# Optimization experiments

Measured on AMD Instinct MI355X. Metric: run time of the kernel, lower is better.

Reference implementation:

```python
import jax, jax.numpy as jnp
import numpy as np

EPS = 1e-5

def batchnorm(x, g, b):
    # training-mode BN: batch statistics over (N,H,W), biased variance (matches torch)
    m = x.mean((0, 2, 3), keepdims=True)
    v = ((x - m) ** 2).mean((0, 2, 3), keepdims=True)
    return g[None, :, None, None] * (x - m) * jax.lax.rsqrt(v + EPS) + b[None, :, None, None]


def deform_conv2d(x, offset, mask, weight, bias):
    # torchvision deform_conv2d v2 semantics, stride=1, pad=1, dilation=1, 1 group, 1 offset group
    B, C, H, W = x.shape
    K = 9  # 3x3 kernel
    off = offset.reshape(B, K, 2, H, W)  # interleaved (dy, dx) per kernel tap
    dy, dx = off[:, :, 0], off[:, :, 1]  # [B,K,H,W]
    kr = jnp.arange(3, dtype=x.dtype) - 1.0
    k_y = jnp.repeat(kr, 3)  # [9] kernel row offsets
    k_x = jnp.tile(kr, 3)    # [9] kernel col offsets
    hh = jnp.arange(H, dtype=x.dtype)
    ww = jnp.arange(W, dtype=x.dtype)
    ph = dy + k_y[None, :, None, None] + hh[None, None, :, None]  # [B,K,H,W] sample rows
    pw = dx + k_x[None, :, None, None] + ww[None, None, None, :]  # [B,K,H,W] sample cols
    h0 = jnp.floor(ph); w0 = jnp.floor(pw)
    lh = ph - h0; lw = pw - w0
    h0i = h0.astype(jnp.int32); w0i = w0.astype(jnp.int32)

    def gather(xb, hb, wb):  # xb [C,H,W], hb/wb [K,H,W] -> [C,K,H,W]
        return xb[:, hb, wb]

    def corner(hi, wi, wgt):
        valid = (hi >= 0) & (hi < H) & (wi >= 0) & (wi < W)
        hic = jnp.clip(hi, 0, H - 1); wic = jnp.clip(wi, 0, W - 1)
        v = jax.vmap(gather)(x, hic, wic)  # [B,C,K,H,W]
        return v * (wgt * valid.astype(x.dtype))[:, None]

    samp = (corner(h0i, w0i, (1 - lh) * (1 - lw))
            + corner(h0i, w0i + 1, (1 - lh) * lw)
            + corner(h0i + 1, w0i, lh * (1 - lw))
            + corner(h0i + 1, w0i + 1, lh * lw))  # [B,C,K,H,W]
    samp = samp * mask[:, None]  # modulated (v2) mask [B,1,K,H,W]
    out = jnp.einsum('bckhw,ock->bohw', samp, weight.reshape(weight.shape[0], C, K))
    return out + bias[None, :, None, None]


def reference(x, conv1_w, bn1_g, bn1_b, off_w, off_b, dcn_w, dcn_b, norm_g, norm_b):
    flip = x[..., ::-1]
    xp = batchnorm(jnp.einsum('bchw,oc->bohw', x, conv1_w), bn1_g, bn1_b)  # 1x1 conv + BN, no relu
    concat = jnp.concatenate([flip, xp], axis=1)  # [B,2C,H,W]
    out = jax.lax.conv_general_dilated(concat, off_w, (1, 1), 'SAME',
                                       dimension_numbers=('NCHW', 'OIHW', 'NCHW'))
    out = out + off_b[None, :, None, None]  # [B,27,H,W]
    o1, o2, mask = jnp.split(out, 3, axis=1)
    offset = jnp.concatenate([o1, o2], axis=1)  # [B,18,H,W]
    mask = jax.nn.sigmoid(mask)  # [B,9,H,W]
    d = deform_conv2d(xp, offset, mask, dcn_w, dcn_b)
    return jax.nn.relu(batchnorm(d, norm_g, norm_b) + xp)


def setup_inputs() -> dict:
    key = jax.random.key(0)
    ks = jax.random.split(key, 6)
    B, C, H, W = 8, 256, 45, 80
    stdv = 1.0 / np.sqrt(C * 9)
    return {
        'x': jax.random.normal(ks[0], (B, C, H, W), jnp.float32),
        'conv1_w': jax.random.normal(ks[1], (C, C), jnp.float32) * 0.05,
        'bn1_g': jnp.ones((C,), jnp.float32),
        'bn1_b': jnp.zeros((C,), jnp.float32),
        'off_w': jax.random.normal(ks[2], (27, 2 * C, 3, 3), jnp.float32) * 0.01,
        'off_b': jax.random.normal(ks[3], (27,), jnp.float32) * 0.01,
        'dcn_w': jax.random.uniform(ks[4], (C, C, 3, 3), jnp.float32, -stdv, stdv),
        'dcn_b': jax.random.normal(ks[5], (C,), jnp.float32) * 0.01,
        'norm_g': jnp.ones((C,), jnp.float32),
        'norm_b': jnp.zeros((C,), jnp.float32),
    }
```

## Files before the change

### kernel.cpp

```cpp
#include <hip/hip_runtime.h>
#include <math.h>

#define BATCH 8
#define CH 256
#define HH 45
#define WW 80
#define HW 3600
#define PTOT 28800

typedef unsigned short u16;
typedef unsigned int   u32;
typedef __attribute__((ext_vector_type(8))) short bf16x8;
typedef __attribute__((ext_vector_type(4))) float f32x4;

struct __align__(8) us4 { u16 x, y, z, w; };

__device__ __forceinline__ u16 bf16_rne(float x) {
  u32 u = __float_as_uint(x);
  u += 0x7FFF + ((u >> 16) & 1);
  return (u16)(u >> 16);
}

__global__ __launch_bounds__(256) void prep_wts(
    const float* __restrict__ conv1_w, const float* __restrict__ off_w,
    const float* __restrict__ dcn_w,
    u16* __restrict__ w1b, u16* __restrict__ wt_offb, u16* __restrict__ wt_b)
{
  int i = blockIdx.x * 256 + threadIdx.x;
  if (i < 256 * 256) {
    w1b[i] = bf16_rne(conv1_w[i]);
  }
  if (i < 9 * 32 * 512) {
    int tap = i >> 14;
    int r   = i & 16383;
    int oc  = r >> 9;
    int c   = r & 511;
    float v = (oc < 27) ? off_w[((size_t)oc * 512 + c) * 9 + tap] : 0.f;
    wt_offb[i] = bf16_rne(v);
  }
  if (i < 9 * 256 * 256) {
    int c = i & 255;
    int oc = (i >> 8) & 255;
    int tap = i >> 16;
    wt_b[i] = bf16_rne(dcn_w[((size_t)oc * 256 + c) * 9 + tap]);
  }
}

__global__ __launch_bounds__(256) void flip_transpose(
    const float* __restrict__ x, u16* __restrict__ concat)
{
  __shared__ float tile[32][36];
  const int b  = blockIdx.z;
  const int c0 = blockIdx.y * 32;
  const int p0 = blockIdx.x * 32;
  int rem = HW - p0; if (rem > 32) rem = 32;
  const int t = threadIdx.x;
  {
    int c = t >> 3, p4 = (t & 7) * 4;
    if (p4 < rem) {
      float4 v = *(const float4*)(x + ((size_t)b * CH + c0 + c) * HW + p0 + p4);
      *(float4*)&tile[c][p4] = v;
    }
  }
  __syncthreads();
  {
    int r = t >> 3, cq = (t & 7) * 4;
    if (r < rem) {
      int p = p0 + r;
      int h = p / WW, w = p - h * WW;
      int pf = h * WW + (WW - 1 - w);
      us4 o;
      o.x = bf16_rne(tile[cq + 0][r]);
      o.y = bf16_rne(tile[cq + 1][r]);
      o.z = bf16_rne(tile[cq + 2][r]);
      o.w = bf16_rne(tile[cq + 3][r]);
      *(us4*)(concat + ((size_t)b * HW + pf) * 512 + c0 + cq) = o;
    }
  }
}

__global__ __launch_bounds__(256) void conv1_mfma(
    const u16* __restrict__ concat, const u16* __restrict__ w1b,
    float* __restrict__ out1)
{
  const int t = threadIdx.x;
  const int wv = t >> 6, lane = t & 63;
  const int lr = lane & 15, lk = lane >> 4;
  const int id = blockIdx.x;
  const int b  = id & 7;
  const int pt = id >> 3;
  const int oc0 = blockIdx.y * 128 + (wv & 1) * 64;
  const int p0  = pt * 128 + (wv >> 1) * 64;

  const u16* bptr[4];
#pragma unroll
  for (int nt = 0; nt < 4; nt++) {
    int pl = p0 + nt * 16 + lr;
    int pc = pl < HW ? pl : HW - 1;
    int h = pc / WW, w = pc - h * WW;
    int pf = b * HW + h * WW + (WW - 1 - w);
    bptr[nt] = concat + (size_t)pf * 512 + lk * 8;
  }
  const u16* aptr = w1b + ((size_t)(oc0 + lr)) * 256 + lk * 8;

  f32x4 acc[4][4];
#pragma unroll
  for (int mt = 0; mt < 4; mt++)
#pragma unroll
    for (int nt = 0; nt < 4; nt++) acc[mt][nt] = (f32x4)0.f;

#pragma unroll
  for (int cc = 0; cc < 8; cc++) {
    bf16x8 af[4], bfv[4];
#pragma unroll
    for (int mt = 0; mt < 4; mt++)
      af[mt] = *(const bf16x8*)(aptr + (size_t)mt * 16 * 256 + cc * 32);
#pragma unroll
    for (int nt = 0; nt < 4; nt++)
      bfv[nt] = *(const bf16x8*)(bptr[nt] + cc * 32);
#pragma unroll
    for (int mt = 0; mt < 4; mt++)
#pragma unroll
      for (int nt = 0; nt < 4; nt++)
        acc[mt][nt] = __builtin_amdgcn_mfma_f32_16x16x32_bf16(
            af[mt], bfv[nt], acc[mt][nt], 0, 0, 0);
  }

#pragma unroll
  for (int mt = 0; mt < 4; mt++) {
    int oc = oc0 + mt * 16 + lk * 4;
#pragma unroll
    for (int nt = 0; nt < 4; nt++) {
      int pl = p0 + nt * 16 + lr;
      if (pl < HW) {
        float* dst = out1 + ((size_t)(b * CH + oc)) * HW + pl;
#pragma unroll
        for (int r = 0; r < 4; r++)
          dst[(size_t)r * HW] = acc[mt][nt][r];
      }
    }
  }
}

__global__ __launch_bounds__(256) void stats_part(
    const float* __restrict__ src, float* __restrict__ part)
{
  const int c = blockIdx.x, b = blockIdx.y;
  const int t = threadIdx.x;
  const float* p = src + ((size_t)b * CH + c) * HW;
  float s = 0.f, s2 = 0.f;
  for (int i = t; i < HW; i += 256) {
    float v = p[i];
    s += v; s2 += v * v;
  }
  __shared__ float ls[256], ls2[256];
  ls[t] = s; ls2[t] = s2;
  __syncthreads();
  for (int off = 128; off > 0; off >>= 1) {
    if (t < off) { ls[t] += ls[t + off]; ls2[t] += ls2[t + off]; }
    __syncthreads();
  }
  if (t == 0) {
    part[((size_t)b * CH + c) * 2]     = ls[0];
    part[((size_t)b * CH + c) * 2 + 1] = ls2[0];
  }
}

__global__ __launch_bounds__(256) void stats_fin(
    const float* __restrict__ part, float* __restrict__ st)
{
  const int c = threadIdx.x;
  float s = 0.f, s2 = 0.f;
#pragma unroll
  for (int b = 0; b < BATCH; b++) {
    s  += part[((size_t)b * CH + c) * 2];
    s2 += part[((size_t)b * CH + c) * 2 + 1];
  }
  float m = s / (float)PTOT;
  float var = s2 / (float)PTOT - m * m;
  st[c] = m;
  st[CH + c] = rsqrtf(var + 1e-5f);
}

__global__ __launch_bounds__(256) void norm_transpose(
    const float* __restrict__ out1, const float* __restrict__ st,
    const float* __restrict__ g, const float* __restrict__ bb,
    u16* __restrict__ concat)
{
  __shared__ float tile[32][36];
  const int b  = blockIdx.z;
  const int c0 = blockIdx.y * 32;
  const int p0 = blockIdx.x * 32;
  int rem = HW - p0; if (rem > 32) rem = 32;
  const int t = threadIdx.x;

  {
    int c  = t >> 3;
    int p4 = (t & 7) * 4;
    int cg = c0 + c;
    float m  = st[cg], rs = st[CH + cg];
    float sc = g[cg] * rs;
    float sh = bb[cg] - m * sc;
    if (p4 < rem) {
      size_t base = ((size_t)b * CH + cg) * HW + p0;
      float4 v = *(const float4*)(out1 + base + p4);
      v.x = v.x * sc + sh; v.y = v.y * sc + sh;
      v.z = v.z * sc + sh; v.w = v.w * sc + sh;
      *(float4*)&tile[c][p4] = v;
    }
  }
  __syncthreads();
  {
    int r  = t >> 3;
    int cq = (t & 7) * 4;
    if (r < rem) {
      us4 o;
      o.x = bf16_rne(tile[cq + 0][r]);
      o.y = bf16_rne(tile[cq + 1][r]);
      o.z = bf16_rne(tile[cq + 2][r]);
      o.w = bf16_rne(tile[cq + 3][r]);
      *(us4*)(concat + ((size_t)b * HW + p0 + r) * 512 + 256 + c0 + cq) = o;
    }
  }
}

__global__ __launch_bounds__(128) void off_mfma(
    const u16* __restrict__ concat, const u16* __restrict__ wt_offb,
    float* __restrict__ offp3)
{
  const int t = threadIdx.x;
  const int g = blockIdx.y;
  const int wv = t >> 6, lane = t & 63;
  const int lr = lane & 15, lk = lane >> 4;
  const int id = blockIdx.x;
  const int b    = id & 7;
  const int tile = id >> 3;
  int pl = tile * 32 + wv * 16 + lr;
  const bool pvalid = pl < HW;
  if (!pvalid) pl = HW - 1;
  const int P = b * HW + pl;
  const int h = pl / WW, w = pl - h * WW;

  f32x4 acc[2];
  acc[0] = (f32x4)0.f; acc[1] = (f32x4)0.f;

#pragma unroll 1
  for (int tl = 0; tl < 3; tl++) {
    int tap = g * 3 + tl;
    int dy = tap / 3 - 1, dx = tap % 3 - 1;
    bool valid = ((unsigned)(h + dy) < HH) && ((unsigned)(w + dx) < WW);
    int Ps = valid ? (P + dy * WW + dx) : P;
    const u16* bp = concat + (size_t)Ps * 512 + lk * 8;
    const u16* ap = wt_offb + ((size_t)tap * 32 + lr) * 512 + lk * 8;
#pragma unroll
    for (int cc = 0; cc < 16; cc++) {
      bf16x8 bfv = *(const bf16x8*)(bp + cc * 32);
      if (!valid) bfv = (bf16x8)(short)0;
      bf16x8 af0 = *(const bf16x8*)(ap + cc * 32);
      bf16x8 af1 = *(const bf16x8*)(ap + 16 * 512 + cc * 32);
      acc[0] = __builtin_amdgcn_mfma_f32_16x16x32_bf16(af0, bfv, acc[0], 0, 0, 0);
      acc[1] = __builtin_amdgcn_mfma_f32_16x16x32_bf16(af1, bfv, acc[1], 0, 0, 0);
    }
  }

  if (pvalid) {
#pragma unroll
    for (int mt = 0; mt < 2; mt++) {
      int oc = mt * 16 + lk * 4;
#pragma unroll
      for (int r = 0; r < 4; r++)
        offp3[((size_t)g * 32 + oc + r) * PTOT + P] = acc[mt][r];
    }
  }
}

__global__ __launch_bounds__(256) void off_finalize(
    const float* __restrict__ offp3, const float* __restrict__ off_b,
    float4* __restrict__ wts4, int4* __restrict__ idx4)
{
  int i = blockIdx.x * 256 + threadIdx.x;
  if (i >= 9 * PTOT) return;
  int k = i / PTOT;
  int P = i - k * PTOT;
  int b = P / HW;
  int p = P - b * HW;
  int h = p / WW;
  int w = p - h * WW;

  float dy = off_b[2 * k], dx = off_b[2 * k + 1], ml = off_b[18 + k];
#pragma unroll
  for (int g = 0; g < 3; g++) {
    const float* base = offp3 + (size_t)g * 32 * PTOT + P;
    dy += base[(size_t)(2 * k    ) * PTOT];
    dx += base[(size_t)(2 * k + 1) * PTOT];
    ml += base[(size_t)(18 + k   ) * PTOT];
  }

  float m = 1.f / (1.f + expf(-ml));
  float ph = dy + (float)(k / 3 - 1) + (float)h;
  float pw = dx + (float)(k % 3 - 1) + (float)w;
  float h0f = floorf(ph), w0f = floorf(pw);
  float lh = ph - h0f, lw = pw - w0f;
  int h0 = (int)h0f, w0 = (int)w0f;
  int h1 = h0 + 1, w1 = w0 + 1;
  float vh0 = (h0 >= 0 && h0 < HH) ? 1.f : 0.f;
  float vh1 = (h1 >= 0 && h1 < HH) ? 1.f : 0.f;
  float vw0 = (w0 >= 0 && w0 < WW) ? 1.f : 0.f;
  float vw1 = (w1 >= 0 && w1 < WW) ? 1.f : 0.f;
  float4 wv;
  wv.x = (1.f - lh) * (1.f - lw) * m * vh0 * vw0;
  wv.y = (1.f - lh) * lw         * m * vh0 * vw1;
  wv.z = lh * (1.f - lw)         * m * vh1 * vw0;
  wv.w = lh * lw                 * m * vh1 * vw1;
  int hc0 = min(max(h0, 0), HH - 1), hc1 = min(max(h1, 0), HH - 1);
  int wc0 = min(max(w0, 0), WW - 1), wc1 = min(max(w1, 0), WW - 1);
  int base = b * HW;
  int4 iv;
  iv.x = (base + hc0 * WW + wc0) * 512 + 256;
  iv.y = (base + hc0 * WW + wc1) * 512 + 256;
  iv.z = (base + hc1 * WW + wc0) * 512 + 256;
  iv.w = (base + hc1 * WW + wc1) * 512 + 256;
  wts4[i] = wv;
  idx4[i] = iv;
}

__global__ __launch_bounds__(512) void deform_mfma(
    const u16* __restrict__ concat,
    const float4* __restrict__ wts4, const int4* __restrict__ idx4,
    const u16* __restrict__ wt_b,
    float* __restrict__ d)
{
  __shared__ u16   samp[64 * 256];
  __shared__ float4 sw4[64];
  __shared__ int4   sidx4[64];

  const int t    = threadIdx.x;
  const int wv   = t >> 6;
  const int lane = t & 63;
  const int lr = lane & 15, lk = lane >> 4;
  const int id   = blockIdx.x;
  const int b    = id & 7;
  const int tile = id >> 3;
  const int P0   = b * HW + tile * 64;
  int lim  = HW - tile * 64;
  if (lim > 64) lim = 64;

  f32x4 acc[2][4];
#pragma unroll
  for (int mt = 0; mt < 2; mt++)
#pragma unroll
    for (int nt = 0; nt < 4; nt++) acc[mt][nt] = (f32x4)0.f;

  const int c4 = lane * 4;

  for (int tap = 0; tap < 9; tap++) {
    __syncthreads();
    if (t < 64) {
      int off = (t < lim) ? t : (lim - 1);
      sw4[t]   = wts4[(size_t)tap * PTOT + P0 + off];
      sidx4[t] = idx4[(size_t)tap * PTOT + P0 + off];
    }
    __syncthreads();

#pragma unroll 2
    for (int it = 0; it < 8; it++) {
      int pos = it * 8 + wv;
      int4  iv = sidx4[pos];
      float4 wq = sw4[pos];
      uint2 u0 = *(const uint2*)(concat + iv.x + c4);
      uint2 u1 = *(const uint2*)(concat + iv.y + c4);
      uint2 u2 = *(const uint2*)(concat + iv.z + c4);
      uint2 u3 = *(const uint2*)(concat + iv.w + c4);
      float a0, a1, a2, a3;
      a0  = wq.x * __uint_as_float(u0.x << 16);
      a1  = wq.x * __uint_as_float(u0.x & 0xFFFF0000u);
      a2  = wq.x * __uint_as_float(u0.y << 16);
      a3  = wq.x * __uint_as_float(u0.y & 0xFFFF0000u);
      a0 = fmaf(wq.y, __uint_as_float(u1.x << 16), a0);
      a1 = fmaf(wq.y, __uint_as_float(u1.x & 0xFFFF0000u), a1);
      a2 = fmaf(wq.y, __uint_as_float(u1.y << 16), a2);
      a3 = fmaf(wq.y, __uint_as_float(u1.y & 0xFFFF0000u), a3);
      a0 = fmaf(wq.z, __uint_as_float(u2.x << 16), a0);
      a1 = fmaf(wq.z, __uint_as_float(u2.x & 0xFFFF0000u), a1);
      a2 = fmaf(wq.z, __uint_as_float(u2.y << 16), a2);
      a3 = fmaf(wq.z, __uint_as_float(u2.y & 0xFFFF0000u), a3);
      a0 = fmaf(wq.w, __uint_as_float(u3.x << 16), a0);
      a1 = fmaf(wq.w, __uint_as_float(u3.x & 0xFFFF0000u), a1);
      a2 = fmaf(wq.w, __uint_as_float(u3.y << 16), a2);
      a3 = fmaf(wq.w, __uint_as_float(u3.y & 0xFFFF0000u), a3);
      uint2 r;
      r.x = (__float_as_uint(a0) >> 16) | (__float_as_uint(a1) & 0xFFFF0000u);
      r.y = (__float_as_uint(a2) >> 16) | (__float_as_uint(a3) & 0xFFFF0000u);
      u32 byte = (u32)pos * 512u + (u32)c4 * 2u;
      byte ^= (u32)(pos & 7) << 4;
      *(uint2*)((char*)samp + byte) = r;
    }
    __syncthreads();

#pragma unroll 1
    for (int cc = 0; cc < 8; cc++) {
      int c0 = cc * 32;
      bf16x8 bfr[4];
#pragma unroll
      for (int nt = 0; nt < 4; nt++) {
        int pos = nt * 16 + lr;
        u32 byte = (u32)pos * 512u + (u32)(c0 + lk * 8) * 2u;
        byte ^= (u32)(pos & 7) << 4;
        bfr[nt] = *(const bf16x8*)((const char*)samp + byte);
      }
      const u16* wp = wt_b + ((size_t)tap * 256 + wv * 32 + lr) * 256
                      + c0 + lk * 8;
      bf16x8 afr[2];
#pragma unroll
      for (int mt = 0; mt < 2; mt++)
        afr[mt] = *(const bf16x8*)(wp + (size_t)mt * 16 * 256);
#pragma unroll
      for (int mt = 0; mt < 2; mt++)
#pragma unroll
        for (int nt = 0; nt < 4; nt++)
          acc[mt][nt] = __builtin_amdgcn_mfma_f32_16x16x32_bf16(
              afr[mt], bfr[nt], acc[mt][nt], 0, 0, 0);
    }
  }

#pragma unroll
  for (int mt = 0; mt < 2; mt++) {
    int oc = wv * 32 + mt * 16 + lk * 4;
#pragma unroll
    for (int nt = 0; nt < 4; nt++) {
      int pl = tile * 64 + nt * 16 + lr;
      if (pl < HW) {
        float* dst = d + ((size_t)(b * CH + oc)) * HW + pl;
#pragma unroll
        for (int r = 0; r < 4; r++)
          dst[(size_t)r * HW] = acc[mt][nt][r];
      }
    }
  }
}

__global__ __launch_bounds__(256) void final_nchw(
    const float* __restrict__ d, const float* __restrict__ out1raw,
    const float* __restrict__ st1, const float* __restrict__ g1,
    const float* __restrict__ b1,
    const float* __restrict__ st2, const float* __restrict__ g2,
    const float* __restrict__ b2, float* __restrict__ out)
{
  u32 i4 = blockIdx.x * 256 + threadIdx.x;
  u32 e = i4 * 4;
  int row = (int)(e / HW);
  int c = row & 255;
  float m1 = st1[c], rs1 = st1[CH + c];
  float sc1 = g1[c] * rs1;
  float sh1 = b1[c] - m1 * sc1;
  float m2 = st2[c], rs2 = st2[CH + c];
  float sc2 = g2[c] * rs2;
  float sh2 = b2[c] - m2 * sc2;
  float4 dv = *(const float4*)(d + e);
  float4 xv = *(const float4*)(out1raw + e);
  float4 o;
  o.x = dv.x * sc2 + sh2 + xv.x * sc1 + sh1;
  o.y = dv.y * sc2 + sh2 + xv.y * sc1 + sh1;
  o.z = dv.z * sc2 + sh2 + xv.z * sc1 + sh1;
  o.w = dv.w * sc2 + sh2 + xv.w * sc1 + sh1;
  o.x = o.x > 0.f ? o.x : 0.f;
  o.y = o.y > 0.f ? o.y : 0.f;
  o.z = o.z > 0.f ? o.z : 0.f;
  o.w = o.w > 0.f ? o.w : 0.f;
  *(float4*)(out + e) = o;
}

extern "C" void kernel_launch(void* const* d_in, const int* in_sizes, int n_in,
                              void* d_out, int out_size, void* d_ws, size_t ws_size,
                              hipStream_t stream)
{
  const float* x       = (const float*)d_in[0];
  const float* conv1_w = (const float*)d_in[1];
  const float* bn1_g   = (const float*)d_in[2];
  const float* bn1_b   = (const float*)d_in[3];
  const float* off_w   = (const float*)d_in[4];
  const float* off_b   = (const float*)d_in[5];
  const float* dcn_w   = (const float*)d_in[6];
  const float* norm_g  = (const float*)d_in[8];
  const float* norm_b  = (const float*)d_in[9];
  float* out = (float*)d_out;

  char* ws = (char*)d_ws;
  size_t o = 0;
  float* out1    = (float*)(ws + o); o += (size_t)PTOT * CH * 4;
  u16*   concat  = (u16*)  (ws + o); o += (size_t)PTOT * 512 * 2;
  float* dbuf    = (float*)(ws + o); o += (size_t)PTOT * CH * 4;
  float* offp3   = (float*)(ws + o); o += (size_t)96 * PTOT * 4;
  u16*   wt_b    = (u16*)  (ws + o); o += (size_t)9 * 256 * 256 * 2;
  u16*   wt_offb = (u16*)  (ws + o); o += (size_t)9 * 32 * 512 * 2;
  u16*   w1b     = (u16*)  (ws + o); o += (size_t)256 * 256 * 2;
  float4* wts4   = (float4*)(ws + o); o += (size_t)9 * PTOT * 16;
  int4*   idx4   = (int4*) (ws + o); o += (size_t)9 * PTOT * 16;
  float* st      = (float*)(ws + o); o += 512 * 4;
  float* st2     = (float*)(ws + o); o += 512 * 4;
  float* part    = (float*)(ws + o); o += (size_t)BATCH * CH * 2 * 4;

  prep_wts<<<2304, 256, 0, stream>>>(conv1_w, off_w, dcn_w, w1b, wt_offb, wt_b);
  flip_transpose<<<dim3(113, 8, 8), 256, 0, stream>>>(x, concat);
  conv1_mfma<<<dim3(232, 2), 256, 0, stream>>>(concat, w1b, out1);
  stats_part<<<dim3(256, 8), 256, 0, stream>>>(out1, part);
  stats_fin<<<1, 256, 0, stream>>>(part, st);
  norm_transpose<<<dim3(113, 8, 8), 256, 0, stream>>>(out1, st, bn1_g, bn1_b, concat);
  off_mfma<<<dim3(904, 3), 128, 0, stream>>>(concat, wt_offb, offp3);
  off_finalize<<<(9 * PTOT + 255) / 256, 256, 0, stream>>>(offp3, off_b, wts4, idx4);
  deform_mfma<<<456, 512, 0, stream>>>(concat, wts4, idx4, wt_b, dbuf);
  stats_part<<<dim3(256, 8), 256, 0, stream>>>(dbuf, part);
  stats_fin<<<1, 256, 0, stream>>>(part, st2);
  final_nchw<<<7200, 256, 0, stream>>>(dbuf, out1, st, bn1_g, bn1_b,
                                       st2, norm_g, norm_b, out);
}
```

Baseline: 281.7 us.

## Warp-specialize deform conv into producer and MFMA consumer waves with double buffering

The deform kernel now runs 12 waves per block: 4 producer waves gather the bilinear samples for the next tap into one of two shared buffers while 8 consumer waves run the MFMA GEMM on the current buffer. This replaces the serial gather, sync, compute sequence per tap, so gather latency is meant to overlap with matrix math. Producers read the per-position weights and indices straight from global memory instead of staging them in shared memory. The larger block and doubled shared buffer raise register and LDS pressure, and only 4 waves now do the gather, so occupancy or gather throughput may become the limit.

```diff
diff --git a/kernel.cpp b/kernel.cpp
--- a/kernel.cpp
+++ b/kernel.cpp
@@ -324,18 +324,16 @@
   idx4[i] = iv;
 }
 
-__global__ __launch_bounds__(512) void deform_mfma(
+__global__ __launch_bounds__(768) void deform_mfma(
     const u16* __restrict__ concat,
     const float4* __restrict__ wts4, const int4* __restrict__ idx4,
     const u16* __restrict__ wt_b,
     float* __restrict__ d)
 {
-  __shared__ u16   samp[64 * 256];
-  __shared__ float4 sw4[64];
-  __shared__ int4   sidx4[64];
+  __shared__ u16 samp[2][64 * 256];
 
   const int t    = threadIdx.x;
-  const int wv   = t >> 6;
+  const int wvid = t >> 6;
   const int lane = t & 63;
   const int lr = lane & 15, lk = lane >> 4;
   const int id   = blockIdx.x;
@@ -345,95 +343,104 @@
   int lim  = HW - tile * 64;
   if (lim > 64) lim = 64;
 
+  const int c4 = lane * 4;
+  const bool producer = (wvid < 4);
+  const int cw = wvid - 4;
+
   f32x4 acc[2][4];
 #pragma unroll
   for (int mt = 0; mt < 2; mt++)
 #pragma unroll
     for (int nt = 0; nt < 4; nt++) acc[mt][nt] = (f32x4)0.f;
 
-  const int c4 = lane * 4;
+#define BUILD(TAP, BUF)                                                        \
+  {                                                                            \
+    _Pragma("unroll 4")                                                        \
+    for (int it = 0; it < 16; it++) {                                          \
+      int pos = it * 4 + wvid;                                                 \
+      int off = pos < lim ? pos : lim - 1;                                     \
+      const int4   iv = idx4[(size_t)(TAP) * PTOT + P0 + off];                 \
+      const float4 wq = wts4[(size_t)(TAP) * PTOT + P0 + off];                 \
+      uint2 u0 = *(const uint2*)(concat + iv.x + c4);                          \
+      uint2 u1 = *(const uint2*)(concat + iv.y + c4);                          \
+      uint2 u2 = *(const uint2*)(concat + iv.z + c4);                          \
+      uint2 u3 = *(const uint2*)(concat + iv.w + c4);                          \
+      float a0, a1, a2, a3;                                                    \
+      a0  = wq.x * __uint_as_float(u0.x << 16);                                \
+      a1  = wq.x * __uint_as_float(u0.x & 0xFFFF0000u);                        \
+      a2  = wq.x * __uint_as_float(u0.y << 16);                                \
+      a3  = wq.x * __uint_as_float(u0.y & 0xFFFF0000u);                        \
+      a0 = fmaf(wq.y, __uint_as_float(u1.x << 16), a0);                        \
+      a1 = fmaf(wq.y, __uint_as_float(u1.x & 0xFFFF0000u), a1);                \
+      a2 = fmaf(wq.y, __uint_as_float(u1.y << 16), a2);                        \
+      a3 = fmaf(wq.y, __uint_as_float(u1.y & 0xFFFF0000u), a3);                \
+      a0 = fmaf(wq.z, __uint_as_float(u2.x << 16), a0);                        \
+      a1 = fmaf(wq.z, __uint_as_float(u2.x & 0xFFFF0000u), a1);                \
+      a2 = fmaf(wq.z, __uint_as_float(u2.y << 16), a2);                        \
+      a3 = fmaf(wq.z, __uint_as_float(u2.y & 0xFFFF0000u), a3);                \
+      a0 = fmaf(wq.w, __uint_as_float(u3.x << 16), a0);                        \
+      a1 = fmaf(wq.w, __uint_as_float(u3.x & 0xFFFF0000u), a1);                \
+      a2 = fmaf(wq.w, __uint_as_float(u3.y << 16), a2);                        \
+      a3 = fmaf(wq.w, __uint_as_float(u3.y & 0xFFFF0000u), a3);                \
+      uint2 r;                                                                 \
+      r.x = (__float_as_uint(a0) >> 16) | (__float_as_uint(a1) & 0xFFFF0000u); \
+      r.y = (__float_as_uint(a2) >> 16) | (__float_as_uint(a3) & 0xFFFF0000u); \
+      u32 byte = (u32)pos * 512u + (u32)c4 * 2u;                               \
+      byte ^= (u32)(pos & 7) << 4;                                             \
+      *(uint2*)((char*)samp[BUF] + byte) = r;                                  \
+    }                                                                          \
+  }
+
+  if (producer) BUILD(0, 0);
+  __syncthreads();
 
   for (int tap = 0; tap < 9; tap++) {
+    const int buf = tap & 1;
+    if (producer) {
+      if (tap < 8) BUILD(tap + 1, buf ^ 1);
+    } else {
+#pragma unroll 1
+      for (int cc = 0; cc < 8; cc++) {
+        int c0 = cc * 32;
+        bf16x8 bfr[4];
+#pragma unroll
+        for (int nt = 0; nt < 4; nt++) {
+          int pos = nt * 16 + lr;
+          u32 byte = (u32)pos * 512u + (u32)(c0 + lk * 8) * 2u;
+          byte ^= (u32)(pos & 7) << 4;
+          bfr[nt] = *(const bf16x8*)((const char*)samp[buf] + byte);
+        }
+        const u16* wp = wt_b + ((size_t)tap * 256 + cw * 32 + lr) * 256
+                        + c0 + lk * 8;
+        bf16x8 afr[2];
+#pragma unroll
+        for (int mt = 0; mt < 2; mt++)
+          afr[mt] = *(const bf16x8*)(wp + (size_t)mt * 16 * 256);
+#pragma unroll
+        for (int mt = 0; mt < 2; mt++)
+#pragma unroll
+          for (int nt = 0; nt < 4; nt++)
+            acc[mt][nt] = __builtin_amdgcn_mfma_f32_16x16x32_bf16(
+                afr[mt], bfr[nt], acc[mt][nt], 0, 0, 0);
+      }
+    }
     __syncthreads();
-    if (t < 64) {
-      int off = (t < lim) ? t : (lim - 1);
-      sw4[t]   = wts4[(size_t)tap * PTOT + P0 + off];
-      sidx4[t] = idx4[(size_t)tap * PTOT + P0 + off];
-    }
-    __syncthreads();
-
-#pragma unroll 2
-    for (int it = 0; it < 8; it++) {
-      int pos = it * 8 + wv;
-      int4  iv = sidx4[pos];
-      float4 wq = sw4[pos];
-      uint2 u0 = *(const uint2*)(concat + iv.x + c4);
-      uint2 u1 = *(const uint2*)(concat + iv.y + c4);
-      uint2 u2 = *(const uint2*)(concat + iv.z + c4);
-      uint2 u3 = *(const uint2*)(concat + iv.w + c4);
-      float a0, a1, a2, a3;
-      a0  = wq.x * __uint_as_float(u0.x << 16);
-      a1  = wq.x * __uint_as_float(u0.x & 0xFFFF0000u);
-      a2  = wq.x * __uint_as_float(u0.y << 16);
-      a3  = wq.x * __uint_as_float(u0.y & 0xFFFF0000u);
-      a0 = fmaf(wq.y, __uint_as_float(u1.x << 16), a0);
-      a1 = fmaf(wq.y, __uint_as_float(u1.x & 0xFFFF0000u), a1);
-      a2 = fmaf(wq.y, __uint_as_float(u1.y << 16), a2);
-      a3 = fmaf(wq.y, __uint_as_float(u1.y & 0xFFFF0000u), a3);
-      a0 = fmaf(wq.z, __uint_as_float(u2.x << 16), a0);
-      a1 = fmaf(wq.z, __uint_as_float(u2.x & 0xFFFF0000u), a1);
-      a2 = fmaf(wq.z, __uint_as_float(u2.y << 16), a2);
-      a3 = fmaf(wq.z, __uint_as_float(u2.y & 0xFFFF0000u), a3);
-      a0 = fmaf(wq.w, __uint_as_float(u3.x << 16), a0);
-      a1 = fmaf(wq.w, __uint_as_float(u3.x & 0xFFFF0000u), a1);
-      a2 = fmaf(wq.w, __uint_as_float(u3.y << 16), a2);
-      a3 = fmaf(wq.w, __uint_as_float(u3.y & 0xFFFF0000u), a3);
-      uint2 r;
-      r.x = (__float_as_uint(a0) >> 16) | (__float_as_uint(a1) & 0xFFFF0000u);
-      r.y = (__float_as_uint(a2) >> 16) | (__float_as_uint(a3) & 0xFFFF0000u);
-      u32 byte = (u32)pos * 512u + (u32)c4 * 2u;
-      byte ^= (u32)(pos & 7) << 4;
-      *(uint2*)((char*)samp + byte) = r;
-    }
-    __syncthreads();
-
-#pragma unroll 1
-    for (int cc = 0; cc < 8; cc++) {
-      int c0 = cc * 32;
-      bf16x8 bfr[4];
+  }
+#undef BUILD
+
+  if (!producer) {
+#pragma unroll
+    for (int mt = 0; mt < 2; mt++) {
+      int oc = cw * 32 + mt * 16 + lk * 4;
 #pragma unroll
       for (int nt = 0; nt < 4; nt++) {
-        int pos = nt * 16 + lr;
-        u32 byte = (u32)pos * 512u + (u32)(c0 + lk * 8) * 2u;
-        byte ^= (u32)(pos & 7) << 4;
-        bfr[nt] = *(const bf16x8*)((const char*)samp + byte);
-      }
-      const u16* wp = wt_b + ((size_t)tap * 256 + wv * 32 + lr) * 256
-                      + c0 + lk * 8;
-      bf16x8 afr[2];
-#pragma unroll
-      for (int mt = 0; mt < 2; mt++)
-        afr[mt] = *(const bf16x8*)(wp + (size_t)mt * 16 * 256);
-#pragma unroll
-      for (int mt = 0; mt < 2; mt++)
-#pragma unroll
-        for (int nt = 0; nt < 4; nt++)
-          acc[mt][nt] = __builtin_amdgcn_mfma_f32_16x16x32_bf16(
-              afr[mt], bfr[nt], acc[mt][nt], 0, 0, 0);
-    }
-  }
-
-#pragma unroll
-  for (int mt = 0; mt < 2; mt++) {
-    int oc = wv * 32 + mt * 16 + lk * 4;
-#pragma unroll
-    for (int nt = 0; nt < 4; nt++) {
-      int pl = tile * 64 + nt * 16 + lr;
-      if (pl < HW) {
-        float* dst = d + ((size_t)(b * CH + oc)) * HW + pl;
-#pragma unroll
-        for (int r = 0; r < 4; r++)
-          dst[(size_t)r * HW] = acc[mt][nt][r];
+        int pl = tile * 64 + nt * 16 + lr;
+        if (pl < HW) {
+          float* dst = d + ((size_t)(b * CH + oc)) * HW + pl;
+#pragma unroll
+          for (int r = 0; r < 4; r++)
+            dst[(size_t)r * HW] = acc[mt][nt][r];
+        }
       }
     }
   }
@@ -508,7 +515,7 @@
   norm_transpose<<<dim3(113, 8, 8), 256, 0, stream>>>(out1, st, bn1_g, bn1_b, concat);
   off_mfma<<<dim3(904, 3), 128, 0, stream>>>(concat, wt_offb, offp3);
   off_finalize<<<(9 * PTOT + 255) / 256, 256, 0, stream>>>(offp3, off_b, wts4, idx4);
-  deform_mfma<<<456, 512, 0, stream>>>(concat, wts4, idx4, wt_b, dbuf);
+  deform_mfma<<<456, 768, 0, stream>>>(concat, wts4, idx4, wt_b, dbuf);
   stats_part<<<dim3(256, 8), 256, 0, stream>>>(dbuf, part);
   stats_fin<<<1, 256, 0, stream>>>(part, st2);
   final_nchw<<<7200, 256, 0, stream>>>(dbuf, out1, st, bn1_g, bn1_b,
```

After: 308.1 us. +9.4%, slower.

## Fuse BN partial statistics into conv1 and deform MFMA epilogues

Applied to the files above, without the earlier changes.

Computes per-channel sum and sum-of-squares directly from the MFMA accumulators in the conv1 and deform kernel epilogues, using lane shuffles and writing per-block partials. This removes the two stats_part passes, which each re-read a full 29 MB fp32 activation tensor. The finalize kernels now run as a single block that serially reduces 464 or 456 partial slots per channel. That is a long serial tail and could offset part of the saving.

```diff
diff --git a/kernel.cpp b/kernel.cpp
--- a/kernel.cpp
+++ b/kernel.cpp
@@ -81,7 +81,7 @@
 
 __global__ __launch_bounds__(256) void conv1_mfma(
     const u16* __restrict__ concat, const u16* __restrict__ w1b,
-    float* __restrict__ out1)
+    float* __restrict__ out1, float* __restrict__ part_c1)
 {
   const int t = threadIdx.x;
   const int wv = t >> 6, lane = t & 63;
@@ -140,41 +140,76 @@
       }
     }
   }
-}
-
-__global__ __launch_bounds__(256) void stats_part(
-    const float* __restrict__ src, float* __restrict__ part)
-{
-  const int c = blockIdx.x, b = blockIdx.y;
-  const int t = threadIdx.x;
-  const float* p = src + ((size_t)b * CH + c) * HW;
+
+  float sv[4][4], sq[4][4];
+#pragma unroll
+  for (int mt = 0; mt < 4; mt++)
+#pragma unroll
+    for (int r = 0; r < 4; r++) { sv[mt][r] = 0.f; sq[mt][r] = 0.f; }
+#pragma unroll
+  for (int mt = 0; mt < 4; mt++)
+#pragma unroll
+    for (int nt = 0; nt < 4; nt++) {
+      int pl = p0 + nt * 16 + lr;
+      if (pl < HW) {
+#pragma unroll
+        for (int r = 0; r < 4; r++) {
+          float v = acc[mt][nt][r];
+          sv[mt][r] += v; sq[mt][r] += v * v;
+        }
+      }
+    }
+#pragma unroll
+  for (int m = 1; m < 16; m <<= 1) {
+#pragma unroll
+    for (int mt = 0; mt < 4; mt++)
+#pragma unroll
+      for (int r = 0; r < 4; r++) {
+        sv[mt][r] += __shfl_xor(sv[mt][r], m, 64);
+        sq[mt][r] += __shfl_xor(sq[mt][r], m, 64);
+      }
+  }
+  if (lr == 0) {
+    int slot = (wv >> 1) + 2 * blockIdx.x + 464 * blockIdx.y;
+    float* pp = part_c1 + (size_t)slot * 128 * 2;
+#pragma unroll
+    for (int mt = 0; mt < 4; mt++)
+#pragma unroll
+      for (int r = 0; r < 4; r++) {
+        int ocl = (wv & 1) * 64 + mt * 16 + lk * 4 + r;
+        pp[ocl * 2]     = sv[mt][r];
+        pp[ocl * 2 + 1] = sq[mt][r];
+      }
+  }
+}
+
+__global__ __launch_bounds__(256) void stats_fin_c1(
+    const float* __restrict__ part_c1, float* __restrict__ st)
+{
+  const int c = threadIdx.x;
+  const int y = c >> 7, ocl = c & 127;
+  const float* base = part_c1 + (size_t)y * 464 * 128 * 2 + ocl * 2;
   float s = 0.f, s2 = 0.f;
-  for (int i = t; i < HW; i += 256) {
-    float v = p[i];
-    s += v; s2 += v * v;
-  }
-  __shared__ float ls[256], ls2[256];
-  ls[t] = s; ls2[t] = s2;
-  __syncthreads();
-  for (int off = 128; off > 0; off >>= 1) {
-    if (t < off) { ls[t] += ls[t + off]; ls2[t] += ls2[t + off]; }
-    __syncthreads();
-  }
-  if (t == 0) {
-    part[((size_t)b * CH + c) * 2]     = ls[0];
-    part[((size_t)b * CH + c) * 2 + 1] = ls2[0];
-  }
-}
-
-__global__ __launch_bounds__(256) void stats_fin(
-    const float* __restrict__ part, float* __restrict__ st)
+#pragma unroll 8
+  for (int i = 0; i < 464; i++) {
+    s  += base[(size_t)i * 256];
+    s2 += base[(size_t)i * 256 + 1];
+  }
+  float m = s / (float)PTOT;
+  float var = s2 / (float)PTOT - m * m;
+  st[c] = m;
+  st[CH + c] = rsqrtf(var + 1e-5f);
+}
+
+__global__ __launch_bounds__(256) void stats_fin_d(
+    const float* __restrict__ part_d, float* __restrict__ st)
 {
   const int c = threadIdx.x;
   float s = 0.f, s2 = 0.f;
-#pragma unroll
-  for (int b = 0; b < BATCH; b++) {
-    s  += part[((size_t)b * CH + c) * 2];
-    s2 += part[((size_t)b * CH + c) * 2 + 1];
+#pragma unroll 8
+  for (int i = 0; i < 456; i++) {
+    s  += part_d[(size_t)i * 512 + c * 2];
+    s2 += part_d[(size_t)i * 512 + c * 2 + 1];
   }
   float m = s / (float)PTOT;
   float var = s2 / (float)PTOT - m * m;
@@ -328,7 +363,7 @@
     const u16* __restrict__ concat,
     const float4* __restrict__ wts4, const int4* __restrict__ idx4,
     const u16* __restrict__ wt_b,
-    float* __restrict__ d)
+    float* __restrict__ d, float* __restrict__ part_d)
 {
   __shared__ u16   samp[64 * 256];
   __shared__ float4 sw4[64];
@@ -437,6 +472,46 @@
       }
     }
   }
+
+  float sv[2][4], sq[2][4];
+#pragma unroll
+  for (int mt = 0; mt < 2; mt++)
+#pragma unroll
+    for (int r = 0; r < 4; r++) { sv[mt][r] = 0.f; sq[mt][r] = 0.f; }
+#pragma unroll
+  for (int mt = 0; mt < 2; mt++)
+#pragma unroll
+    for (int nt = 0; nt < 4; nt++) {
+      int pl = tile * 64 + nt * 16 + lr;
+      if (pl < HW) {
+#pragma unroll
+        for (int r = 0; r < 4; r++) {
+          float v = acc[mt][nt][r];
+          sv[mt][r] += v; sq[mt][r] += v * v;
+        }
+      }
+    }
+#pragma unroll
+  for (int m = 1; m < 16; m <<= 1) {
+#pragma unroll
+    for (int mt = 0; mt < 2; mt++)
+#pragma unroll
+      for (int r = 0; r < 4; r++) {
+        sv[mt][r] += __shfl_xor(sv[mt][r], m, 64);
+        sq[mt][r] += __shfl_xor(sq[mt][r], m, 64);
+      }
+  }
+  if (lr == 0) {
+    float* pp = part_d + (size_t)blockIdx.x * 512;
+#pragma unroll
+    for (int mt = 0; mt < 2; mt++)
+#pragma unroll
+      for (int r = 0; r < 4; r++) {
+        int oc = wv * 32 + mt * 16 + lk * 4 + r;
+        pp[oc * 2]     = sv[mt][r];
+        pp[oc * 2 + 1] = sq[mt][r];
+      }
+  }
 }
 
 __global__ __launch_bounds__(256) void final_nchw(
@@ -498,19 +573,18 @@
   int4*   idx4   = (int4*) (ws + o); o += (size_t)9 * PTOT * 16;
   float* st      = (float*)(ws + o); o += 512 * 4;
   float* st2     = (float*)(ws + o); o += 512 * 4;
-  float* part    = (float*)(ws + o); o += (size_t)BATCH * CH * 2 * 4;
+  float* part_c1 = (float*)(ws + o); o += (size_t)928 * 128 * 2 * 4;
+  float* part_d  = (float*)(ws + o); o += (size_t)456 * 512 * 4;
 
   prep_wts<<<2304, 256, 0, stream>>>(conv1_w, off_w, dcn_w, w1b, wt_offb, wt_b);
   flip_transpose<<<dim3(113, 8, 8), 256, 0, stream>>>(x, concat);
-  conv1_mfma<<<dim3(232, 2), 256, 0, stream>>>(concat, w1b, out1);
-  stats_part<<<dim3(256, 8), 256, 0, stream>>>(out1, part);
-  stats_fin<<<1, 256, 0, stream>>>(part, st);
+  conv1_mfma<<<dim3(232, 2), 256, 0, stream>>>(concat, w1b, out1, part_c1);
+  stats_fin_c1<<<1, 256, 0, stream>>>(part_c1, st);
   norm_transpose<<<dim3(113, 8, 8), 256, 0, stream>>>(out1, st, bn1_g, bn1_b, concat);
   off_mfma<<<dim3(904, 3), 128, 0, stream>>>(concat, wt_offb, offp3);
   off_finalize<<<(9 * PTOT + 255) / 256, 256, 0, stream>>>(offp3, off_b, wts4, idx4);
-  deform_mfma<<<456, 512, 0, stream>>>(concat, wts4, idx4, wt_b, dbuf);
-  stats_part<<<dim3(256, 8), 256, 0, stream>>>(dbuf, part);
-  stats_fin<<<1, 256, 0, stream>>>(part, st2);
+  deform_mfma<<<456, 512, 0, stream>>>(concat, wts4, idx4, wt_b, dbuf, part_d);
+  stats_fin_d<<<1, 256, 0, stream>>>(part_d, st2);
   final_nchw<<<7200, 256, 0, stream>>>(dbuf, out1, st, bn1_g, bn1_b,
                                        st2, norm_g, norm_b, out);
 }
```

Result: slower. 309.3 us (+9.8%).
